# Kernel tuning notes

Hardware: AMD Instinct MI355X
Metric: run time of the kernel (lower is better)

The kernel has to match this reference:

```python
import jax, jax.numpy as jnp
import numpy as np

IFZ = 256      # in_features
SFZ = 1280     # sequence_features
AHZ = 8        # attention heads
AFZ = 64       # attention feature dim per head
NRES = 20      # canonical_num_residues
SCALE = float(np.sqrt(AFZ))
RESID = float(np.sqrt(2.0))
EPS = 1e-6


def _ln(x, s, b, eps=1e-5):
    m = jnp.mean(x, axis=-1, keepdims=True)
    v = jnp.var(x, axis=-1, keepdims=True)
    return (x - m) / jnp.sqrt(v + eps) * s + b


def setup_inputs() -> dict:
    key = jax.random.key(0)
    ks = jax.random.split(key, 20)
    N, B, S = 4096, 4, 512
    HD = AHZ * AFZ
    w = lambda k, shp: (jax.random.normal(k, shp, jnp.float32) * 0.02)
    d = {}
    d["x"] = jax.random.normal(ks[0], (N, IFZ), jnp.float32)
    d["packed_sequence_emb"] = jax.random.normal(ks[1], (B, S, SFZ), jnp.float32)
    d["packed_sequence_mask"] = jnp.ones((B, S), jnp.float32)
    d["prot_mask"] = jnp.arange(N, dtype=jnp.int32)
    d["batch"] = jax.random.randint(ks[2], (N,), 0, B, jnp.int32)
    # projections (bias=False)
    d["Wq"] = w(ks[3], (HD, IFZ))
    d["Wk"] = w(ks[4], (HD, SFZ))
    d["Wv"] = w(ks[5], (HD, SFZ))
    # ag: LayerNorm(HD) -> Linear(HD, IFZ, bias=False) (dropout = identity at eval)
    d["ag_ln_s"] = jnp.ones((HD,), jnp.float32)
    d["ag_ln_b"] = jnp.zeros((HD,), jnp.float32)
    d["Wag"] = w(ks[6], (IFZ, HD))
    d["res_ln_s"] = jnp.ones((3, IFZ), jnp.float32)
    d["res_ln_b"] = jnp.zeros((3, IFZ), jnp.float32)
    d["res_w1"] = w(ks[7], (3, IFZ, IFZ))
    d["res_b1"] = jnp.zeros((3, IFZ), jnp.float32)
    d["res_w2"] = w(ks[8], (3, IFZ, IFZ))
    d["res_b2"] = jnp.zeros((3, IFZ), jnp.float32)
    d["head_w"] = w(ks[9], (NRES, IFZ))
    d["head_b"] = jnp.zeros((NRES,), jnp.float32)
    # output LayerNorm en
    d["en_s"] = jnp.ones((IFZ,), jnp.float32)
    d["en_b"] = jnp.zeros((IFZ,), jnp.float32)
    return d


def _forward(x, emb, mask, prot_mask, batch, Wq, Wk, Wv, ag_ln_s, ag_ln_b, Wag,
             res_ln_s, res_ln_b, res_w1, res_b1, res_w2, res_b2,
             head_w, head_b, en_s, en_b):
    N = x.shape[0]
    B, S = emb.shape[:2]
    b_idx = batch[prot_mask]                      # [M]
    xp = x[prot_mask]                             # [M, IFZ]
    M = xp.shape[0]
    q = (xp @ Wq.T).reshape(M, AHZ, AFZ)          # [M,H,D]
    k = (emb @ Wk.T).reshape(B, S, AHZ, AFZ)      # [B,S,H,D]
    v = (emb @ Wv.T).reshape(B, S, AHZ, AFZ)
    # score vs every protein, then pick own protein (avoids materializing [M,S,H,D] gather)
    scores_all = jnp.einsum('mhd,bshd->mbsh', q, k) / SCALE          # [M,B,S,H]
    sel = b_idx[:, None, None, None]
    scores = jnp.take_along_axis(scores_all, sel, axis=1)[:, 0]       # [M,S,H]
    mb = mask[b_idx][:, :, None]                                      # [M,S,1]
    # padded_sequence_softmax: softmax over S, zero pads, renormalize
    sm = jax.nn.softmax(scores, axis=1) * mb
    w = sm / (jnp.sum(sm, axis=1, keepdims=True) + EPS)               # [M,S,H]
    feat_all = jnp.einsum('msh,bshd->mbhd', w, v)                     # [M,B,H,D]
    feat = jnp.take_along_axis(feat_all, sel, axis=1)[:, 0]
    feat = feat.reshape(M, AHZ * AFZ)
    ag = _ln(feat, ag_ln_s, ag_ln_b) @ Wag.T                          # [M, IFZ]
    # seq_aa_head on the scattered new features (identical to ag for unique prot_mask)
    h = ag
    for i in range(3):
        y = _ln(h, res_ln_s[i], res_ln_b[i])
        y = jax.nn.relu(y @ res_w1[i].T + res_b1[i])
        y = y @ res_w2[i].T + res_b2[i]
        h = (h + y) / RESID
    logits = h @ head_w.T + head_b                                     # [M, NRES]
    new_features = jnp.zeros_like(x).at[prot_mask].set(ag)
    seq_aa_logits = jnp.zeros((N, NRES), x.dtype).at[prot_mask].set(logits)
    unpacked_scores = jnp.zeros((N, S, AHZ), x.dtype).at[prot_mask].set(scores)
    out_x = _ln(x + new_features / RESID, en_s, en_b)
    return out_x, seq_aa_logits, unpacked_scores


def reference(x, packed_sequence_emb, packed_sequence_mask, prot_mask, batch,
              Wq, Wk, Wv, ag_ln_s, ag_ln_b, Wag,
              res_ln_s, res_ln_b, res_w1, res_b1, res_w2, res_b2,
              head_w, head_b, en_s, en_b):
    return _forward(x, packed_sequence_emb, packed_sequence_mask, prot_mask, batch,
                    Wq, Wk, Wv, ag_ln_s, ag_ln_b, Wag,
                    res_ln_s, res_ln_b, res_w1, res_b1, res_w2, res_b2,
                    head_w, head_b, en_s, en_b)
```

## Files before the change

kernel.cpp:

```cpp
#include <hip/hip_runtime.h>
#include <math.h>


typedef short bf8 __attribute__((ext_vector_type(8)));
typedef float f32x4 __attribute__((ext_vector_type(4)));
typedef unsigned short u16;

constexpr int LDT = 40;
enum { EPI_NONE = 0, EPI_BIAS_RELU = 1, EPI_BIAS = 2, EPI_RESID = 3 };
#define RSQRT2 0.70710678118654752f

__device__ __forceinline__ u16 f2bf(float f) {
  unsigned int u = __builtin_bit_cast(unsigned int, f);
  unsigned int r = u + 0x7fffu + ((u >> 16) & 1u);
  return (u16)(r >> 16);
}
__device__ __forceinline__ float bf2f(u16 v) {
  return __builtin_bit_cast(float, (unsigned int)v << 16);
}
__device__ __forceinline__ f32x4 mfma16(bf8 a, bf8 b, f32x4 c) {
  return __builtin_amdgcn_mfma_f32_16x16x32_bf16(a, b, c, 0, 0, 0);
}

struct CvtDesc { const float* src; u16* dst; int n; };
struct CvtArgs { CvtDesc d[8]; };

__global__ __launch_bounds__(256) void cvt_k(CvtArgs a) {
  CvtDesc d = a.d[blockIdx.z];
  int i = (blockIdx.x * 256 + threadIdx.x) * 8;
  if (i >= d.n) return;
  f32x4 v0 = *(const f32x4*)(d.src + i);
  f32x4 v1 = *(const f32x4*)(d.src + i + 4);
  bf8 o;
  o[0] = (short)f2bf(v0[0]); o[1] = (short)f2bf(v0[1]);
  o[2] = (short)f2bf(v0[2]); o[3] = (short)f2bf(v0[3]);
  o[4] = (short)f2bf(v1[0]); o[5] = (short)f2bf(v1[1]);
  o[6] = (short)f2bf(v1[2]); o[7] = (short)f2bf(v1[3]);
  *(bf8*)(d.dst + i) = o;
}

template <int EPI, bool BFOUT>
__global__ __launch_bounds__(256) void mgemm2(
    const u16* __restrict__ A, const u16* __restrict__ B,
    void* __restrict__ Cv, int M, int N, int K, int lda, int ldb, int ldc,
    const float* __restrict__ bias, const float* __restrict__ Hin,
    const int* __restrict__ gatherA, const int* __restrict__ scatterC) {
  __shared__ __align__(16) u16 As[128 * LDT];
  __shared__ __align__(16) u16 Bs[64 * LDT];
  const int tid = threadIdx.x;
  const int m0 = blockIdx.y * 128, n0 = blockIdx.x * 64;
  const int wave = tid >> 6, lane = tid & 63;
  const int wm = (wave & 1) * 64, wn = (wave >> 1) * 32;
  const int lrow = lane & 15, quad = lane >> 4;
  const int srow = tid >> 2, skq = tid & 3;

  int gr0 = m0 + srow, gr1 = m0 + srow + 64;
  int ar0 = (gr0 < M) ? (gatherA ? gatherA[gr0] : gr0) : -1;
  int ar1 = (gr1 < M) ? (gatherA ? gatherA[gr1] : gr1) : -1;
  const u16* Ap0 = (ar0 >= 0) ? A + (size_t)ar0 * lda + skq * 8 : nullptr;
  const u16* Ap1 = (ar1 >= 0) ? A + (size_t)ar1 * lda + skq * 8 : nullptr;
  const u16* Bp = (n0 + srow < N) ? B + (size_t)(n0 + srow) * ldb + skq * 8 : nullptr;
  u16* AsW0 = &As[srow * LDT + skq * 8];
  u16* AsW1 = &As[(srow + 64) * LDT + skq * 8];
  u16* BsW = &Bs[srow * LDT + skq * 8];

  f32x4 acc[4][2];
#pragma unroll
  for (int i = 0; i < 4; ++i)
#pragma unroll
    for (int j = 0; j < 2; ++j) acc[i][j] = (f32x4){0.f, 0.f, 0.f, 0.f};
  const bf8 z8 = {0, 0, 0, 0, 0, 0, 0, 0};

  for (int k0 = 0; k0 < K; k0 += 32) {
    bf8 a0 = Ap0 ? *(const bf8*)(Ap0 + k0) : z8;
    bf8 a1 = Ap1 ? *(const bf8*)(Ap1 + k0) : z8;
    bf8 bv = Bp ? *(const bf8*)(Bp + k0) : z8;
    *(bf8*)AsW0 = a0;
    *(bf8*)AsW1 = a1;
    *(bf8*)BsW = bv;
    __syncthreads();
    bf8 af[4], bfr[2];
#pragma unroll
    for (int i = 0; i < 4; ++i)
      af[i] = *(const bf8*)&As[(wm + i * 16 + lrow) * LDT + quad * 8];
#pragma unroll
    for (int j = 0; j < 2; ++j)
      bfr[j] = *(const bf8*)&Bs[(wn + j * 16 + lrow) * LDT + quad * 8];
#pragma unroll
    for (int i = 0; i < 4; ++i)
#pragma unroll
      for (int j = 0; j < 2; ++j) acc[i][j] = mfma16(af[i], bfr[j], acc[i][j]);
    __syncthreads();
  }

  float* Cf = (float*)Cv;
  u16* Cb = (u16*)Cv;
#pragma unroll
  for (int i = 0; i < 4; ++i) {
#pragma unroll
    for (int r = 0; r < 4; ++r) {
      int row = m0 + wm + i * 16 + quad * 4 + r;
      if (row >= M) continue;
      if (gatherA && gatherA[row] < 0) continue;
      int orow = scatterC ? scatterC[row] : row;
#pragma unroll
      for (int j = 0; j < 2; ++j) {
        int col = n0 + wn + j * 16 + lrow;
        if (col >= N) continue;
        float v = acc[i][j][r];
        if (EPI == EPI_BIAS_RELU) v = fmaxf(v + bias[col], 0.f);
        else if (EPI == EPI_BIAS) v += bias[col];
        else if (EPI == EPI_RESID) v = (Hin[(size_t)row * ldc + col] + v + bias[col]) * RSQRT2;
        if (BFOUT) Cb[(size_t)orow * ldc + col] = f2bf(v);
        else Cf[(size_t)orow * ldc + col] = v;
      }
    }
  }
}

__global__ __launch_bounds__(256) void vtrans(const u16* __restrict__ KV,
                                              u16* __restrict__ VT) {
  __shared__ u16 t[32][33];
  int b = blockIdx.z;
  int s0 = blockIdx.x * 32, d0 = blockIdx.y * 32;
  int tx = threadIdx.x & 31, ty = threadIdx.x >> 5;
#pragma unroll
  for (int i = 0; i < 32; i += 8)
    t[ty + i][tx] = KV[(size_t)(b * 512 + s0 + ty + i) * 1024 + 512 + d0 + tx];
  __syncthreads();
#pragma unroll
  for (int i = 0; i < 32; i += 8)
    VT[(size_t)(b * 512 + d0 + ty + i) * 512 + s0 + tx] = t[tx][ty + i];
}

constexpr int WST = 520;
constexpr int QST = 72;

__global__ __launch_bounds__(256) void attn_fused(
    const u16* __restrict__ Q, const u16* __restrict__ KV,
    const u16* __restrict__ VT, const int* __restrict__ list,
    const float* __restrict__ mask, u16* __restrict__ packed,
    u16* __restrict__ feat, int N) {
  const int b = blockIdx.y >> 3, h = blockIdx.y & 7;
  const int mt = blockIdx.x;
  const int* lst = list + (size_t)b * N + mt * 32;
  if (lst[0] < 0) return;

  __shared__ __align__(16) u16 Ws[32 * WST];
  __shared__ __align__(16) u16 Qs[32 * QST];
  __shared__ __align__(16) u16 KVs[64 * QST];
  __shared__ __align__(16) float mk[8][68];
  __shared__ int mS[32];

  const int tid = threadIdx.x;
  const int wave = tid >> 6, lane = tid & 63;
  const int wm = (wave & 1) * 16, wns = (wave >> 1) * 32;
  const int lrow = lane & 15, quad = lane >> 4;
  const bf8 z8 = {0, 0, 0, 0, 0, 0, 0, 0};

  if (tid < 32) mS[tid] = lst[tid];
  {
    int p = tid >> 5, j = (tid & 31) * 2;
    *(float2*)&mk[p][j] = *(const float2*)&mask[(size_t)b * 512 + p * 64 + j];
  }
  {
    int qr = tid >> 3, kq = tid & 7;
    int m = lst[qr];
    *(bf8*)&Qs[qr * QST + kq * 8] =
        (m >= 0) ? *(const bf8*)(Q + (size_t)m * 512 + h * 64 + kq * 8) : z8;
  }
  __syncthreads();

  const bf8 qa0 = *(const bf8*)&Qs[(wm + lrow) * QST + 0 + quad * 8];
  const bf8 qa1 = *(const bf8*)&Qs[(wm + lrow) * QST + 32 + quad * 8];

  const u16* KVb = KV + (size_t)(b * 512) * 1024 + h * 64;
  for (int st = 0; st < 8; ++st) {
    const int sta = (st + mt) & 7;
#pragma unroll
    for (int i = 0; i < 2; ++i) {
      int c = tid * 2 + i;
      int sr = c >> 3, kq = c & 7;
      *(bf8*)&KVs[sr * QST + kq * 8] =
          *(const bf8*)(KVb + (size_t)(sta * 64 + sr) * 1024 + kq * 8);
    }
    __syncthreads();
    f32x4 acc0 = {0.f, 0.f, 0.f, 0.f}, acc1 = acc0;
    {
      bf8 b00 = *(const bf8*)&KVs[(wns + lrow) * QST + quad * 8];
      bf8 b10 = *(const bf8*)&KVs[(wns + 16 + lrow) * QST + quad * 8];
      bf8 b01 = *(const bf8*)&KVs[(wns + lrow) * QST + 32 + quad * 8];
      bf8 b11 = *(const bf8*)&KVs[(wns + 16 + lrow) * QST + 32 + quad * 8];
      acc0 = mfma16(qa0, b00, acc0);
      acc1 = mfma16(qa0, b10, acc1);
      acc0 = mfma16(qa1, b01, acc0);
      acc1 = mfma16(qa1, b11, acc1);
    }
#pragma unroll
    for (int r = 0; r < 4; ++r) {
      int lr = wm + quad * 4 + r;
      Ws[lr * WST + sta * 64 + wns + lrow] = f2bf(acc0[r] * 0.125f);
      Ws[lr * WST + sta * 64 + wns + 16 + lrow] = f2bf(acc1[r] * 0.125f);
    }
    __syncthreads();
  }

  {
    const int row = tid >> 3, part = tid & 7;
    u16* wrow = &Ws[row * WST + part * 64];
    const int mm = mS[row];
    bf8 w[8];
    float mx = -1e30f;
#pragma unroll
    for (int v = 0; v < 8; ++v) {
      w[v] = *(const bf8*)(wrow + v * 8);
#pragma unroll
      for (int j = 0; j < 8; ++j) mx = fmaxf(mx, bf2f((u16)w[v][j]));
    }
    if (mm >= 0) {
      u16* prow = packed + ((size_t)h * N + mm) * 512 + part * 64;
#pragma unroll
      for (int v = 0; v < 8; ++v) *(bf8*)(prow + v * 8) = w[v];
    }
#pragma unroll
    for (int d = 1; d < 8; d <<= 1) mx = fmaxf(mx, __shfl_xor(mx, d));
    float ev[64];
    float se = 0.f, ms = 0.f;
#pragma unroll
    for (int v = 0; v < 8; ++v) {
      f32x4 m0 = *(const f32x4*)&mk[part][v * 8];
      f32x4 m1 = *(const f32x4*)&mk[part][v * 8 + 4];
#pragma unroll
      for (int j = 0; j < 8; ++j) {
        float e = __expf(bf2f((u16)w[v][j]) - mx);
        ev[v * 8 + j] = e;
        se += e;
        ms += e * (j < 4 ? m0[j] : m1[j - 4]);
      }
    }
#pragma unroll
    for (int d = 1; d < 8; d <<= 1) {
      se += __shfl_xor(se, d);
      ms += __shfl_xor(ms, d);
    }
    float iv = 1.0f / (ms + 1e-6f * se);
#pragma unroll
    for (int v = 0; v < 8; ++v) {
      f32x4 m0 = *(const f32x4*)&mk[part][v * 8];
      f32x4 m1 = *(const f32x4*)&mk[part][v * 8 + 4];
      bf8 o;
#pragma unroll
      for (int j = 0; j < 8; ++j)
        o[j] = (short)f2bf(ev[v * 8 + j] * (j < 4 ? m0[j] : m1[j - 4]) * iv);
      *(bf8*)(wrow + v * 8) = o;
    }
  }
  __syncthreads();

  f32x4 acc0 = {0.f, 0.f, 0.f, 0.f}, acc1 = acc0;
  const u16* VTb = VT + (size_t)(b * 512 + h * 64) * 512;
  for (int ss = 0; ss < 8; ++ss) {
    const int s0 = ((ss + mt) & 7) << 6;
#pragma unroll
    for (int i = 0; i < 2; ++i) {
      int c = tid * 2 + i;
      int sr = c >> 3, kq = c & 7;
      *(bf8*)&KVs[sr * QST + kq * 8] =
          *(const bf8*)(VTb + (size_t)sr * 512 + s0 + kq * 8);
    }
    __syncthreads();
#pragma unroll
    for (int k0 = 0; k0 < 64; k0 += 32) {
      bf8 a = *(const bf8*)&Ws[(wm + lrow) * WST + s0 + k0 + quad * 8];
      bf8 b0 = *(const bf8*)&KVs[(wns + lrow) * QST + k0 + quad * 8];
      bf8 b1 = *(const bf8*)&KVs[(wns + 16 + lrow) * QST + k0 + quad * 8];
      acc0 = mfma16(a, b0, acc0);
      acc1 = mfma16(a, b1, acc1);
    }
    __syncthreads();
  }
#pragma unroll
  for (int r = 0; r < 4; ++r) {
    int lr = wm + quad * 4 + r;
    int mm = mS[lr];
    if (mm < 0) continue;
    u16* frow = feat + (size_t)mm * 512 + h * 64;
    frow[wns + lrow] = f2bf(acc0[r]);
    frow[wns + 16 + lrow] = f2bf(acc1[r]);
  }
}

__global__ __launch_bounds__(256) void unpack_k(const u16* __restrict__ packed,
                                                const int* __restrict__ pm,
                                                float* __restrict__ out_sc,
                                                int N) {
  __shared__ u16 Ls[8 * 520];
  int m = blockIdx.x, tid = threadIdx.x;
  int h = tid >> 5, c = (tid & 31) * 16;
  const u16* row = packed + ((size_t)h * N + m) * 512 + c;
  *(bf8*)&Ls[h * 520 + c] = *(const bf8*)row;
  *(bf8*)&Ls[h * 520 + c + 8] = *(const bf8*)(row + 8);
  __syncthreads();
  float* orow = out_sc + (size_t)pm[m] * 4096;
#pragma unroll
  for (int i = 0; i < 16; ++i) {
    int e = tid + i * 256;
    orow[e] = bf2f(Ls[(e & 7) * 520 + (e >> 3)]);
  }
}

constexpr int HST = 268;
constexpr int AST = 520;
constexpr int YST = 280;

__global__ __launch_bounds__(512) void mlp_fused(
    const u16* __restrict__ feat, const float* __restrict__ ag_s,
    const float* __restrict__ ag_b, const u16* __restrict__ Wag,
    float* __restrict__ AGout, const float* __restrict__ rls,
    const float* __restrict__ rlb, const u16* __restrict__ rw1,
    const float* __restrict__ rb1, const u16* __restrict__ rw2,
    const float* __restrict__ rb2, const float* __restrict__ hw,
    const float* __restrict__ hb, const int* __restrict__ pm,
    float* __restrict__ out_lg) {
  __shared__ __align__(16) float Hs[16 * HST];
  __shared__ __align__(16) u16 As[16 * AST];
  __shared__ __align__(16) u16 Ys[16 * YST];
  const int tid = threadIdx.x;
  const int m0 = blockIdx.x * 8;
  const int wave = tid >> 6, lane = tid & 63;
  const int lrow = lane & 15, quad = lane >> 4;
  const int wn = wave * 32;
  const int row = tid >> 5, part = tid & 31;
  const int rot16 = blockIdx.x & 15, rot8 = blockIdx.x & 7;

  {
    const u16* frow = feat + (size_t)(m0 + (row & 7)) * 512 + part * 16;
    bf8 f0 = *(const bf8*)frow;
    bf8 f1 = *(const bf8*)(frow + 8);
    float s = 0.f, sq = 0.f;
#pragma unroll
    for (int j = 0; j < 8; ++j) {
      float a = bf2f((u16)f0[j]), b = bf2f((u16)f1[j]);
      s += a + b;
      sq += a * a + b * b;
    }
#pragma unroll
    for (int d = 1; d < 32; d <<= 1) { s += __shfl_xor(s, d); sq += __shfl_xor(sq, d); }
    float mean = s * (1.0f / 512.0f);
    float var = sq * (1.0f / 512.0f) - mean * mean;
    float is = 1.0f / sqrtf(var + 1e-5f);
    int c = part * 16;
    bf8 o0, o1;
#pragma unroll
    for (int j = 0; j < 8; ++j) {
      o0[j] = (short)f2bf((bf2f((u16)f0[j]) - mean) * is * ag_s[c + j] + ag_b[c + j]);
      o1[j] = (short)f2bf((bf2f((u16)f1[j]) - mean) * is * ag_s[c + 8 + j] + ag_b[c + 8 + j]);
    }
    *(bf8*)&As[row * AST + c] = o0;
    *(bf8*)&As[row * AST + c + 8] = o1;
  }
  __syncthreads();

  {
    f32x4 acc0 = {0.f, 0.f, 0.f, 0.f}, acc1 = acc0;
#pragma unroll 4
    for (int kk = 0; kk < 16; ++kk) {
      int k0 = ((kk + rot16) & 15) << 5;
      bf8 a = *(const bf8*)&As[lrow * AST + k0 + quad * 8];
      bf8 w0 = *(const bf8*)&Wag[(size_t)(wn + lrow) * 512 + k0 + quad * 8];
      bf8 w1 = *(const bf8*)&Wag[(size_t)(wn + 16 + lrow) * 512 + k0 + quad * 8];
      acc0 = mfma16(a, w0, acc0);
      acc1 = mfma16(a, w1, acc1);
    }
#pragma unroll
    for (int r = 0; r < 4; ++r) {
      int rr = quad * 4 + r;
      Hs[rr * HST + wn + lrow] = acc0[r];
      Hs[rr * HST + wn + 16 + lrow] = acc1[r];
      if (rr < 8) {
        AGout[(size_t)(m0 + rr) * 256 + wn + lrow] = acc0[r];
        AGout[(size_t)(m0 + rr) * 256 + wn + 16 + lrow] = acc1[r];
      }
    }
  }

  for (int layer = 0; layer < 3; ++layer) {
    __syncthreads();
    {
      int c = part * 8;
      f32x4 h0 = *(const f32x4*)&Hs[row * HST + c];
      f32x4 h1 = *(const f32x4*)&Hs[row * HST + c + 4];
      float s = 0.f, sq = 0.f;
#pragma unroll
      for (int e = 0; e < 4; ++e) {
        s += h0[e] + h1[e];
        sq += h0[e] * h0[e] + h1[e] * h1[e];
      }
#pragma unroll
      for (int d = 1; d < 32; d <<= 1) { s += __shfl_xor(s, d); sq += __shfl_xor(sq, d); }
      float mean = s * (1.0f / 256.0f);
      float var = sq * (1.0f / 256.0f) - mean * mean;
      float is = 1.0f / sqrtf(var + 1e-5f);
      const float* g = rls + layer * 256;
      const float* bb = rlb + layer * 256;
      bf8 o;
#pragma unroll
      for (int e = 0; e < 4; ++e) {
        o[e] = (short)f2bf((h0[e] - mean) * is * g[c + e] + bb[c + e]);
        o[e + 4] = (short)f2bf((h1[e] - mean) * is * g[c + 4 + e] + bb[c + 4 + e]);
      }
      *(bf8*)&As[row * AST + c] = o;
    }
    __syncthreads();

    {
      const u16* W = rw1 + (size_t)layer * 65536;
      f32x4 acc0 = {0.f, 0.f, 0.f, 0.f}, acc1 = acc0;
#pragma unroll 4
      for (int kk = 0; kk < 8; ++kk) {
        int k0 = ((kk + rot8) & 7) << 5;
        bf8 a = *(const bf8*)&As[lrow * AST + k0 + quad * 8];
        bf8 w0 = *(const bf8*)&W[(size_t)(wn + lrow) * 256 + k0 + quad * 8];
        bf8 w1 = *(const bf8*)&W[(size_t)(wn + 16 + lrow) * 256 + k0 + quad * 8];
        acc0 = mfma16(a, w0, acc0);
        acc1 = mfma16(a, w1, acc1);
      }
      const float* b1 = rb1 + layer * 256;
      float bi0 = b1[wn + lrow], bi1 = b1[wn + 16 + lrow];
#pragma unroll
      for (int r = 0; r < 4; ++r) {
        int rr = quad * 4 + r;
        Ys[rr * YST + wn + lrow] = f2bf(fmaxf(acc0[r] + bi0, 0.f));
        Ys[rr * YST + wn + 16 + lrow] = f2bf(fmaxf(acc1[r] + bi1, 0.f));
      }
    }
    __syncthreads();

    {
      const u16* W = rw2 + (size_t)layer * 65536;
      f32x4 acc0 = {0.f, 0.f, 0.f, 0.f}, acc1 = acc0;
#pragma unroll 4
      for (int kk = 0; kk < 8; ++kk) {
        int k0 = ((kk + rot8) & 7) << 5;
        bf8 a = *(const bf8*)&Ys[lrow * YST + k0 + quad * 8];
        bf8 w0 = *(const bf8*)&W[(size_t)(wn + lrow) * 256 + k0 + quad * 8];
        bf8 w1 = *(const bf8*)&W[(size_t)(wn + 16 + lrow) * 256 + k0 + quad * 8];
        acc0 = mfma16(a, w0, acc0);
        acc1 = mfma16(a, w1, acc1);
      }
      const float* b2 = rb2 + layer * 256;
      float bi0 = b2[wn + lrow], bi1 = b2[wn + 16 + lrow];
#pragma unroll
      for (int r = 0; r < 4; ++r) {
        int rr = quad * 4 + r;
        float* h0 = &Hs[rr * HST + wn + lrow];
        float* h1 = &Hs[rr * HST + wn + 16 + lrow];
        *h0 = (*h0 + acc0[r] + bi0) * RSQRT2;
        *h1 = (*h1 + acc1[r] + bi1) * RSQRT2;
      }
    }
  }
  __syncthreads();

  if (row < 8 && part < 20) {
    const float* hrow = &Hs[row * HST];
    const float* wrow = hw + (size_t)part * 256;
    float l0 = 0.f, l1 = 0.f, l2 = 0.f, l3 = 0.f;
    for (int k = 0; k < 256; k += 16) {
      f32x4 h0 = *(const f32x4*)&hrow[k];
      f32x4 h1 = *(const f32x4*)&hrow[k + 4];
      f32x4 h2 = *(const f32x4*)&hrow[k + 8];
      f32x4 h3 = *(const f32x4*)&hrow[k + 12];
      f32x4 w0 = *(const f32x4*)&wrow[k];
      f32x4 w1 = *(const f32x4*)&wrow[k + 4];
      f32x4 w2 = *(const f32x4*)&wrow[k + 8];
      f32x4 w3 = *(const f32x4*)&wrow[k + 12];
#pragma unroll
      for (int e = 0; e < 4; ++e) {
        l0 += h0[e] * w0[e];
        l1 += h1[e] * w1[e];
        l2 += h2[e] * w2[e];
        l3 += h3[e] * w3[e];
      }
    }
    out_lg[(size_t)pm[m0 + row] * 20 + part] = l0 + l1 + l2 + l3 + hb[part];
  }
}

__global__ __launch_bounds__(256) void outx_k(
    const float* __restrict__ x, const float* __restrict__ ag,
    const int* __restrict__ inv, const float* __restrict__ g,
    const float* __restrict__ bb, float* __restrict__ out) {
  __shared__ float red[256];
  int n = blockIdx.x, tid = threadIdx.x;
  int mi = inv[n];
  float v = x[(size_t)n * 256 + tid];
  if (mi >= 0) v += ag[(size_t)mi * 256 + tid] * RSQRT2;
  red[tid] = v;
  __syncthreads();
  for (int off = 128; off; off >>= 1) {
    if (tid < off) red[tid] += red[tid + off];
    __syncthreads();
  }
  float mean = red[0] * (1.0f / 256.0f);
  __syncthreads();
  red[tid] = v * v;
  __syncthreads();
  for (int off = 128; off; off >>= 1) {
    if (tid < off) red[tid] += red[tid + off];
    __syncthreads();
  }
  float var = red[0] * (1.0f / 256.0f) - mean * mean;
  float is = 1.0f / sqrtf(var + 1e-5f);
  out[(size_t)n * 256 + tid] = (v - mean) * is * g[tid] + bb[tid];
}

__global__ void init_idx_k(int* __restrict__ list, int* __restrict__ inv,
                           int* __restrict__ cnt, int N, int B) {
  int i = blockIdx.x * 256 + threadIdx.x;
  if (i < B * N) list[i] = -1;
  if (i < N) inv[i] = -1;
  if (i < B) cnt[i] = 0;
}

__global__ void compact_k(const int* __restrict__ pm,
                          const int* __restrict__ batch, int* __restrict__ list,
                          int* __restrict__ inv, int* __restrict__ cnt, int N) {
  int m = blockIdx.x * 256 + threadIdx.x;
  if (m >= N) return;
  int p = pm[m];
  int b = batch[p];
  int slot = atomicAdd(&cnt[b], 1);
  list[(size_t)b * N + slot] = m;
  inv[p] = m;
}

extern "C" void kernel_launch(void* const* d_in, const int* in_sizes, int n_in,
                              void* d_out, int out_size, void* d_ws,
                              size_t ws_size, hipStream_t stream) {
  const float* x = (const float*)d_in[0];
  const float* emb = (const float*)d_in[1];
  const float* mask = (const float*)d_in[2];
  const int* pm = (const int*)d_in[3];
  const int* batch = (const int*)d_in[4];
  const float* Wq = (const float*)d_in[5];
  const float* Wk = (const float*)d_in[6];
  const float* Wv = (const float*)d_in[7];
  const float* ag_s = (const float*)d_in[8];
  const float* ag_b = (const float*)d_in[9];
  const float* Wag = (const float*)d_in[10];
  const float* rls = (const float*)d_in[11];
  const float* rlb = (const float*)d_in[12];
  const float* rw1 = (const float*)d_in[13];
  const float* rb1 = (const float*)d_in[14];
  const float* rw2 = (const float*)d_in[15];
  const float* rb2 = (const float*)d_in[16];
  const float* hw = (const float*)d_in[17];
  const float* hb = (const float*)d_in[18];
  const float* ens = (const float*)d_in[19];
  const float* enb = (const float*)d_in[20];

  const int N = in_sizes[0] / 256;
  const int B = in_sizes[2] / 512;

  char* wsb = (char*)d_ws;
  u16* embbf = (u16*)(wsb + 0);
  u16* xbf   = (u16*)(wsb + 5242880);
  u16* Wkvbf = (u16*)(wsb + 7340032);
  u16* Wqbf  = (u16*)(wsb + 9961472);
  u16* packed = (u16*)(wsb + 0);
  u16* KVbf   = (u16*)(wsb + 33554432);
  u16* Qbf    = (u16*)(wsb + 37748736);
  u16* VT     = (u16*)(wsb + 41943040);
  u16* featE  = (u16*)(wsb + 44040192);
  float* AG = (float*)(wsb + 37748736);
  u16* Wagbf = (u16*)(wsb + 48234496);
  u16* rw1bf = (u16*)(wsb + 48496640);
  u16* rw2bf = (u16*)(wsb + 48889856);
  int* list  = (int*)(wsb + 49545216);
  int* inv   = (int*)(wsb + 49610752);
  int* cnt   = (int*)(wsb + 49627136);

  float* out_x = (float*)d_out;
  float* out_lg = out_x + (size_t)N * 256;
  float* out_sc = out_lg + (size_t)N * 20;

  CvtArgs ca;
  ca.d[0] = {emb, embbf, 2 * 512 * 1280 * 2};
  ca.d[1] = {x, xbf, 4096 * 256};
  ca.d[2] = {Wk, Wkvbf, 512 * 1280};
  ca.d[3] = {Wv, Wkvbf + 512 * 1280, 512 * 1280};
  ca.d[4] = {Wq, Wqbf, 512 * 256};
  ca.d[5] = {Wag, Wagbf, 256 * 512};
  ca.d[6] = {rw1, rw1bf, 3 * 256 * 256};
  ca.d[7] = {rw2, rw2bf, 3 * 256 * 256};
  cvt_k<<<dim3(1281, 1, 8), 256, 0, stream>>>(ca);
  init_idx_k<<<(B * N + 255) / 256, 256, 0, stream>>>(list, inv, cnt, N, B);
  compact_k<<<(N + 255) / 256, 256, 0, stream>>>(pm, batch, list, inv, cnt, N);

  mgemm2<EPI_NONE, true><<<dim3(16, 16), 256, 0, stream>>>(
      embbf, Wkvbf, KVbf, B * 512, 1024, 1280, 1280, 1280, 1024,
      nullptr, nullptr, nullptr, nullptr);
  mgemm2<EPI_NONE, true><<<dim3(8, 32), 256, 0, stream>>>(
      xbf, Wqbf, Qbf, N, 512, 256, 256, 256, 512,
      nullptr, nullptr, pm, nullptr);
  vtrans<<<dim3(16, 16, B), 256, 0, stream>>>(KVbf, VT);

  attn_fused<<<dim3(N / 32, B * 8), 256, 0, stream>>>(
      Qbf, KVbf, VT, list, mask, packed, featE, N);
  unpack_k<<<N, 256, 0, stream>>>(packed, pm, out_sc, N);

  mlp_fused<<<dim3(N / 8), 512, 0, stream>>>(
      featE, ag_s, ag_b, Wagbf, AG, rls, rlb, rw1bf, rb1, rw2bf, rb2,
      hw, hb, pm, out_lg);

  outx_k<<<N, 256, 0, stream>>>(x, AG, inv, ens, enb, out_x);
}
```

Measured before the change: 336.8 us.

## Process 16 rows per MLP block with 16 waves each owning a 16-column slice

```diff
diff --git a/kernel.cpp b/kernel.cpp
--- a/kernel.cpp
+++ b/kernel.cpp
@@ -3,6 +3,7 @@
 
 
 typedef short bf8 __attribute__((ext_vector_type(8)));
+typedef short bf4 __attribute__((ext_vector_type(4)));
 typedef float f32x4 __attribute__((ext_vector_type(4)));
 typedef unsigned short u16;
 
@@ -313,7 +314,7 @@
 constexpr int AST = 520;
 constexpr int YST = 280;
 
-__global__ __launch_bounds__(512) void mlp_fused(
+__global__ __launch_bounds__(1024) void mlp_fused(
     const u16* __restrict__ feat, const float* __restrict__ ag_s,
     const float* __restrict__ ag_b, const u16* __restrict__ Wag,
     float* __restrict__ AGout, const float* __restrict__ rls,
@@ -326,145 +327,115 @@
   __shared__ __align__(16) u16 As[16 * AST];
   __shared__ __align__(16) u16 Ys[16 * YST];
   const int tid = threadIdx.x;
-  const int m0 = blockIdx.x * 8;
+  const int m0 = blockIdx.x * 16;
   const int wave = tid >> 6, lane = tid & 63;
   const int lrow = lane & 15, quad = lane >> 4;
-  const int wn = wave * 32;
-  const int row = tid >> 5, part = tid & 31;
-  const int rot16 = blockIdx.x & 15, rot8 = blockIdx.x & 7;
+  const int wn = wave * 16;
+  const int row = wave;
 
   {
-    const u16* frow = feat + (size_t)(m0 + (row & 7)) * 512 + part * 16;
+    const u16* frow = feat + (size_t)(m0 + row) * 512 + lane * 8;
     bf8 f0 = *(const bf8*)frow;
-    bf8 f1 = *(const bf8*)(frow + 8);
     float s = 0.f, sq = 0.f;
 #pragma unroll
     for (int j = 0; j < 8; ++j) {
-      float a = bf2f((u16)f0[j]), b = bf2f((u16)f1[j]);
-      s += a + b;
-      sq += a * a + b * b;
-    }
-#pragma unroll
-    for (int d = 1; d < 32; d <<= 1) { s += __shfl_xor(s, d); sq += __shfl_xor(sq, d); }
+      float a = bf2f((u16)f0[j]);
+      s += a;
+      sq += a * a;
+    }
+#pragma unroll
+    for (int d = 1; d < 64; d <<= 1) { s += __shfl_xor(s, d); sq += __shfl_xor(sq, d); }
     float mean = s * (1.0f / 512.0f);
     float var = sq * (1.0f / 512.0f) - mean * mean;
     float is = 1.0f / sqrtf(var + 1e-5f);
-    int c = part * 16;
-    bf8 o0, o1;
-#pragma unroll
-    for (int j = 0; j < 8; ++j) {
+    int c = lane * 8;
+    bf8 o0;
+#pragma unroll
+    for (int j = 0; j < 8; ++j)
       o0[j] = (short)f2bf((bf2f((u16)f0[j]) - mean) * is * ag_s[c + j] + ag_b[c + j]);
-      o1[j] = (short)f2bf((bf2f((u16)f1[j]) - mean) * is * ag_s[c + 8 + j] + ag_b[c + 8 + j]);
-    }
     *(bf8*)&As[row * AST + c] = o0;
-    *(bf8*)&As[row * AST + c + 8] = o1;
   }
   __syncthreads();
 
   {
-    f32x4 acc0 = {0.f, 0.f, 0.f, 0.f}, acc1 = acc0;
+    f32x4 acc = {0.f, 0.f, 0.f, 0.f};
 #pragma unroll 4
-    for (int kk = 0; kk < 16; ++kk) {
-      int k0 = ((kk + rot16) & 15) << 5;
+    for (int k0 = 0; k0 < 512; k0 += 32) {
       bf8 a = *(const bf8*)&As[lrow * AST + k0 + quad * 8];
-      bf8 w0 = *(const bf8*)&Wag[(size_t)(wn + lrow) * 512 + k0 + quad * 8];
-      bf8 w1 = *(const bf8*)&Wag[(size_t)(wn + 16 + lrow) * 512 + k0 + quad * 8];
-      acc0 = mfma16(a, w0, acc0);
-      acc1 = mfma16(a, w1, acc1);
+      bf8 w = *(const bf8*)&Wag[(size_t)(wn + lrow) * 512 + k0 + quad * 8];
+      acc = mfma16(a, w, acc);
     }
 #pragma unroll
     for (int r = 0; r < 4; ++r) {
       int rr = quad * 4 + r;
-      Hs[rr * HST + wn + lrow] = acc0[r];
-      Hs[rr * HST + wn + 16 + lrow] = acc1[r];
-      if (rr < 8) {
-        AGout[(size_t)(m0 + rr) * 256 + wn + lrow] = acc0[r];
-        AGout[(size_t)(m0 + rr) * 256 + wn + 16 + lrow] = acc1[r];
-      }
+      Hs[rr * HST + wn + lrow] = acc[r];
+      AGout[(size_t)(m0 + rr) * 256 + wn + lrow] = acc[r];
     }
   }
 
   for (int layer = 0; layer < 3; ++layer) {
     __syncthreads();
     {
-      int c = part * 8;
+      int c = lane * 4;
       f32x4 h0 = *(const f32x4*)&Hs[row * HST + c];
-      f32x4 h1 = *(const f32x4*)&Hs[row * HST + c + 4];
-      float s = 0.f, sq = 0.f;
-#pragma unroll
-      for (int e = 0; e < 4; ++e) {
-        s += h0[e] + h1[e];
-        sq += h0[e] * h0[e] + h1[e] * h1[e];
-      }
-#pragma unroll
-      for (int d = 1; d < 32; d <<= 1) { s += __shfl_xor(s, d); sq += __shfl_xor(sq, d); }
+      float s = h0[0] + h0[1] + h0[2] + h0[3];
+      float sq = h0[0] * h0[0] + h0[1] * h0[1] + h0[2] * h0[2] + h0[3] * h0[3];
+#pragma unroll
+      for (int d = 1; d < 64; d <<= 1) { s += __shfl_xor(s, d); sq += __shfl_xor(sq, d); }
       float mean = s * (1.0f / 256.0f);
       float var = sq * (1.0f / 256.0f) - mean * mean;
       float is = 1.0f / sqrtf(var + 1e-5f);
       const float* g = rls + layer * 256;
       const float* bb = rlb + layer * 256;
-      bf8 o;
-#pragma unroll
-      for (int e = 0; e < 4; ++e) {
+      bf4 o;
+#pragma unroll
+      for (int e = 0; e < 4; ++e)
         o[e] = (short)f2bf((h0[e] - mean) * is * g[c + e] + bb[c + e]);
-        o[e + 4] = (short)f2bf((h1[e] - mean) * is * g[c + 4 + e] + bb[c + 4 + e]);
-      }
-      *(bf8*)&As[row * AST + c] = o;
+      *(bf4*)&As[row * AST + c] = o;
     }
     __syncthreads();
 
     {
       const u16* W = rw1 + (size_t)layer * 65536;
-      f32x4 acc0 = {0.f, 0.f, 0.f, 0.f}, acc1 = acc0;
+      f32x4 acc = {0.f, 0.f, 0.f, 0.f};
 #pragma unroll 4
-      for (int kk = 0; kk < 8; ++kk) {
-        int k0 = ((kk + rot8) & 7) << 5;
+      for (int k0 = 0; k0 < 256; k0 += 32) {
         bf8 a = *(const bf8*)&As[lrow * AST + k0 + quad * 8];
-        bf8 w0 = *(const bf8*)&W[(size_t)(wn + lrow) * 256 + k0 + quad * 8];
-        bf8 w1 = *(const bf8*)&W[(size_t)(wn + 16 + lrow) * 256 + k0 + quad * 8];
-        acc0 = mfma16(a, w0, acc0);
-        acc1 = mfma16(a, w1, acc1);
-      }
-      const float* b1 = rb1 + layer * 256;
-      float bi0 = b1[wn + lrow], bi1 = b1[wn + 16 + lrow];
+        bf8 w = *(const bf8*)&W[(size_t)(wn + lrow) * 256 + k0 + quad * 8];
+        acc = mfma16(a, w, acc);
+      }
+      float bi = rb1[layer * 256 + wn + lrow];
 #pragma unroll
       for (int r = 0; r < 4; ++r) {
         int rr = quad * 4 + r;
-        Ys[rr * YST + wn + lrow] = f2bf(fmaxf(acc0[r] + bi0, 0.f));
-        Ys[rr * YST + wn + 16 + lrow] = f2bf(fmaxf(acc1[r] + bi1, 0.f));
+        Ys[rr * YST + wn + lrow] = f2bf(fmaxf(acc[r] + bi, 0.f));
       }
     }
     __syncthreads();
 
     {
       const u16* W = rw2 + (size_t)layer * 65536;
-      f32x4 acc0 = {0.f, 0.f, 0.f, 0.f}, acc1 = acc0;
+      f32x4 acc = {0.f, 0.f, 0.f, 0.f};
 #pragma unroll 4
-      for (int kk = 0; kk < 8; ++kk) {
-        int k0 = ((kk + rot8) & 7) << 5;
+      for (int k0 = 0; k0 < 256; k0 += 32) {
         bf8 a = *(const bf8*)&Ys[lrow * YST + k0 + quad * 8];
-        bf8 w0 = *(const bf8*)&W[(size_t)(wn + lrow) * 256 + k0 + quad * 8];
-        bf8 w1 = *(const bf8*)&W[(size_t)(wn + 16 + lrow) * 256 + k0 + quad * 8];
-        acc0 = mfma16(a, w0, acc0);
-        acc1 = mfma16(a, w1, acc1);
-      }
-      const float* b2 = rb2 + layer * 256;
-      float bi0 = b2[wn + lrow], bi1 = b2[wn + 16 + lrow];
+        bf8 w = *(const bf8*)&W[(size_t)(wn + lrow) * 256 + k0 + quad * 8];
+        acc = mfma16(a, w, acc);
+      }
+      float bi = rb2[layer * 256 + wn + lrow];
 #pragma unroll
       for (int r = 0; r < 4; ++r) {
         int rr = quad * 4 + r;
         float* h0 = &Hs[rr * HST + wn + lrow];
-        float* h1 = &Hs[rr * HST + wn + 16 + lrow];
-        *h0 = (*h0 + acc0[r] + bi0) * RSQRT2;
-        *h1 = (*h1 + acc1[r] + bi1) * RSQRT2;
-      }
-    }
-  }
-  __syncthreads();
-
-  if (row < 8 && part < 20) {
+        *h0 = (*h0 + acc[r] + bi) * RSQRT2;
+      }
+    }
+  }
+  __syncthreads();
+
+  if (lane < 20) {
     const float* hrow = &Hs[row * HST];
-    const float* wrow = hw + (size_t)part * 256;
+    const float* wrow = hw + (size_t)lane * 256;
     float l0 = 0.f, l1 = 0.f, l2 = 0.f, l3 = 0.f;
     for (int k = 0; k < 256; k += 16) {
       f32x4 h0 = *(const f32x4*)&hrow[k];
@@ -483,7 +454,7 @@
         l3 += h3[e] * w3[e];
       }
     }
-    out_lg[(size_t)pm[m0 + row] * 20 + part] = l0 + l1 + l2 + l3 + hb[part];
+    out_lg[(size_t)pm[m0 + row] * 20 + lane] = l0 + l1 + l2 + l3 + hb[lane];
   }
 }
 
@@ -610,7 +581,7 @@
       Qbf, KVbf, VT, list, mask, packed, featE, N);
   unpack_k<<<N, 256, 0, stream>>>(packed, pm, out_sc, N);
 
-  mlp_fused<<<dim3(N / 8), 512, 0, stream>>>(
+  mlp_fused<<<dim3(N / 16), 1024, 0, stream>>>(
       featE, ag_s, ag_b, Wagbf, AG, rls, rlb, rw1bf, rb1, rw2bf, rb2,
       hw, hb, pm, out_lg);
 
```

New measurement: 313.0 us. 1.08x faster.
